# Kernel tuning notes

Measured on AMD Instinct MI355X. Metric: run time of the kernel, lower is better.

## Reference

```python
import math
import jax, jax.numpy as jnp
import numpy as np

B, S, H, D = 8, 2048, 16, 80
DM = H * D  # 1280 = input_dims


def setup_inputs() -> dict:
    key = jax.random.key(0)
    ks = jax.random.split(key, 10)
    s = 0.02
    return {
        "x": jax.random.normal(ks[0], (B, S, DM), dtype=jnp.float32),
        "Wq": jax.random.normal(ks[1], (DM, DM), dtype=jnp.float32) * s,
        "bq": jnp.zeros((DM,), dtype=jnp.float32),
        "Wk": jax.random.normal(ks[2], (DM, DM), dtype=jnp.float32) * s,
        "bk": jnp.zeros((DM,), dtype=jnp.float32),
        "Wv": jax.random.normal(ks[3], (DM, DM), dtype=jnp.float32) * s,
        "bv": jnp.zeros((DM,), dtype=jnp.float32),
        "Wp": jax.random.normal(ks[4], (DM, DM), dtype=jnp.float32) * s,
        "bp": jnp.zeros((DM,), dtype=jnp.float32),
        "per_dim_scale": jnp.ones((D,), dtype=jnp.float32),
    }


def reference(x, Wq, bq, Wk, bk, Wv, bv, Wp, bp, per_dim_scale):
    # Projections: [B,S,DM] -> [B,S,H,D]
    q = (x @ Wq + bq).reshape(B, S, H, D)
    k = (x @ Wk + bk).reshape(B, S, H, D)
    v = (x @ Wv + bv).reshape(B, S, H, D)
    # Faithful to source: matmul over last two dims of (B,S,H,D) tensors,
    # i.e. scores are [B,S,H,H] -- mixing across HEADS at each position.
    scale = 1.0 / math.sqrt(D)
    attn = jnp.einsum('bshd,bstd->bsht', q, k) * scale  # [B,S,H,H]
    attn = jax.nn.softmax(attn, axis=-1)
    out = jnp.einsum('bsht,bstd->bshd', attn, v)  # [B,S,H,D]
    out = out * per_dim_scale  # broadcast over D
    out = out.reshape(B, S, DM)
    return out @ Wp + bp
```

## Files before the change

### kernel.cpp

```cpp
#include <hip/hip_runtime.h>
#include <hip/hip_bf16.h>

#define M_TOT   16384
#define DMODEL  1280
#define NHEAD   16
#define DHEAD   80
#define NTC     5
#define BK      64
#define NKT     (DMODEL / BK)

typedef __attribute__((ext_vector_type(8))) __bf16 bf16x8;
typedef __attribute__((ext_vector_type(4))) float  f32x4;

__device__ __forceinline__ void gload16(const void* g, void* l) {
  __builtin_amdgcn_global_load_lds(
      (const __attribute__((address_space(1))) void*)g,
      (__attribute__((address_space(3))) void*)l, 16, 0, 0);
}

__device__ __forceinline__ float bf2f(unsigned short u) {
  return __uint_as_float((unsigned)u << 16);
}

__global__ __launch_bounds__(256) void cvt_bf16_kernel(
    const float* __restrict__ x, __hip_bfloat16* __restrict__ y, int n4) {
  int i = blockIdx.x * 256 + threadIdx.x;
  if (i >= n4) return;
  float4 v = ((const float4*)x)[i];
  union { ushort4 u; __hip_bfloat16 h[4]; } o;
  o.h[0] = __float2bfloat16(v.x);
  o.h[1] = __float2bfloat16(v.y);
  o.h[2] = __float2bfloat16(v.z);
  o.h[3] = __float2bfloat16(v.w);
  ((ushort4*)y)[i] = o.u;
}

__global__ __launch_bounds__(256) void transpose_cvt_kernel(
    const float* __restrict__ W0, const float* __restrict__ W1,
    const float* __restrict__ W2, const float* __restrict__ W3,
    const float* __restrict__ pds,
    __hip_bfloat16* __restrict__ T0, __hip_bfloat16* __restrict__ T1,
    __hip_bfloat16* __restrict__ T2, __hip_bfloat16* __restrict__ T3) {
  const float* W = blockIdx.z == 0 ? W0 : blockIdx.z == 1 ? W1
                 : blockIdx.z == 2 ? W2 : W3;
  __hip_bfloat16* T = blockIdx.z == 0 ? T0 : blockIdx.z == 1 ? T1
                    : blockIdx.z == 2 ? T2 : T3;
  __shared__ float tile[32][33];
  int bx = blockIdx.x * 32, by = blockIdx.y * 32;
  int tx = threadIdx.x, ty = threadIdx.y;
  for (int j = 0; j < 32; j += 8)
    tile[ty + j][tx] = W[(size_t)(by + ty + j) * DMODEL + bx + tx];
  __syncthreads();
  const float scale = (blockIdx.z == 3) ? pds[(by + tx) % DHEAD] : 1.0f;
  for (int j = 0; j < 32; j += 8)
    T[(size_t)(bx + ty + j) * DMODEL + by + tx] =
        __float2bfloat16(tile[tx][ty + j] * scale);
}

#define MFMA16(AF, BF, MB)                                                   \
  do {                                                                       \
    _Pragma("unroll")                                                        \
    for (int j_ = 0; j_ < 4; ++j_) {                                         \
      _Pragma("unroll")                                                      \
      for (int n_ = 0; n_ < 4; ++n_)                                         \
        acc[(MB) + j_][n_] = __builtin_amdgcn_mfma_f32_16x16x32_bf16(        \
            AF[j_], BF[n_], acc[(MB) + j_][n_], 0, 0, 0);                    \
    }                                                                        \
  } while (0)

#define PHASE_TAIL()                                                         \
  __builtin_amdgcn_sched_barrier(0);                                         \
  __builtin_amdgcn_s_barrier();                                              \
  asm volatile("s_waitcnt lgkmcnt(0)" ::: "memory");                         \
  __builtin_amdgcn_sched_barrier(0)

#define PHASE_END()                                                          \
  __builtin_amdgcn_sched_barrier(0);                                         \
  __builtin_amdgcn_s_barrier()

template <bool OUT_BF16>
__global__ __launch_bounds__(512, 2) void gemm_bt_kernel(
    const __hip_bfloat16* __restrict__ A,
    const __hip_bfloat16* __restrict__ Bt0,
    const __hip_bfloat16* __restrict__ Bt1,
    const __hip_bfloat16* __restrict__ Bt2,
    const float* __restrict__ bias0, const float* __restrict__ bias1,
    const float* __restrict__ bias2,
    void* __restrict__ C0, void* __restrict__ C1, void* __restrict__ C2) {
  const int mat   = blockIdx.y / NTC;
  const int ntile = blockIdx.y % NTC;
  const __hip_bfloat16* Bt = mat == 0 ? Bt0 : mat == 1 ? Bt1 : Bt2;
  const float* bias        = mat == 0 ? bias0 : mat == 1 ? bias1 : bias2;
  void* C                  = mat == 0 ? C0 : mat == 1 ? C1 : C2;

  const int bm = blockIdx.x * 256;
  const int bn = ntile * 256;

  __shared__ __align__(16) char SLDS[131072];

  const int tid  = threadIdx.x;
  const int lane = tid & 63;
  const int wid  = tid >> 6;
  const int wm   = (wid >> 2) * 128;
  const int wn   = (wid & 3) * 64;
  const int lrow = lane & 15;
  const int l4   = lane >> 4;

  const int rsub  = lane >> 2;
  const int cswz  = (lane & 3) ^ ((rsub >> 1) & 3);
  const char* gsrc[2][2][2];
#pragma unroll
  for (int i = 0; i < 2; ++i) {
    const int rA = bm + wid * 32 + i * 16 + rsub;
    const int rB = bn + wid * 32 + i * 16 + rsub;
#pragma unroll
    for (int s = 0; s < 2; ++s) {
      gsrc[0][i][s] = (const char*)A  + (size_t)rA * (DMODEL * 2) + s * 64 + cswz * 16;
      gsrc[1][i][s] = (const char*)Bt + (size_t)rB * (DMODEL * 2) + s * 64 + cswz * 16;
    }
  }

  auto issueGroup = [&](int M, int s, int nbuf, size_t koff) {
    char* d = SLDS + M * 65536 + nbuf * 32768 + s * 16384 + wid * 2048;
    gload16(gsrc[M][0][s] + koff, d);
    gload16(gsrc[M][1][s] + koff, d + 1024);
  };

  f32x4 acc[8][4];
#pragma unroll
  for (int i = 0; i < 8; ++i)
#pragma unroll
    for (int j = 0; j < 4; ++j) acc[i][j] = (f32x4){0.f, 0.f, 0.f, 0.f};

  const int swz  = ((l4 ^ ((lrow >> 1) & 3)) << 4);
  const int aOff = (wm + lrow) * 64 + swz;
  const int bOff = 65536 + (wn + lrow) * 64 + swz;

  issueGroup(0, 0, 0, 0);
  issueGroup(1, 0, 0, 0);
  issueGroup(0, 1, 0, 0);
  issueGroup(1, 1, 0, 0);
  asm volatile("s_waitcnt vmcnt(4)" ::: "memory");
  __builtin_amdgcn_s_barrier();

  for (int t = 0; t < NKT; ++t) {
    const int buf = t & 1, nbuf = buf ^ 1;
    const int b0 = buf << 15;
    const size_t koff = (size_t)(t + 1) * (BK * 2);
    const bool pf = (t + 1 < NKT);

    bf16x8 aF[4], aG[4], bF[4];

#pragma unroll
    for (int j = 0; j < 4; ++j)
      aF[j] = *(const bf16x8*)(const void*)(SLDS + b0 + aOff + j * 1024);
#pragma unroll
    for (int n = 0; n < 4; ++n)
      bF[n] = *(const bf16x8*)(const void*)(SLDS + b0 + bOff + n * 1024);
    if (pf) issueGroup(0, 0, nbuf, koff);
    PHASE_TAIL();
    __builtin_amdgcn_s_setprio(1);
    MFMA16(aF, bF, 0);
    __builtin_amdgcn_s_setprio(0);
    PHASE_END();

#pragma unroll
    for (int j = 0; j < 4; ++j)
      aG[j] = *(const bf16x8*)(const void*)(SLDS + b0 + aOff + (4 + j) * 1024);
    if (pf) {
      issueGroup(1, 0, nbuf, koff);
      asm volatile("s_waitcnt vmcnt(4)" ::: "memory");
    } else {
      asm volatile("s_waitcnt vmcnt(0)" ::: "memory");
    }
    PHASE_TAIL();
    __builtin_amdgcn_s_setprio(1);
    MFMA16(aG, bF, 4);
    __builtin_amdgcn_s_setprio(0);
    PHASE_END();

#pragma unroll
    for (int j = 0; j < 4; ++j)
      aF[j] = *(const bf16x8*)(const void*)(SLDS + b0 + 16384 + aOff + j * 1024);
#pragma unroll
    for (int n = 0; n < 4; ++n)
      bF[n] = *(const bf16x8*)(const void*)(SLDS + b0 + 16384 + bOff + n * 1024);
    if (pf) issueGroup(0, 1, nbuf, koff);
    PHASE_TAIL();
    __builtin_amdgcn_s_setprio(1);
    MFMA16(aF, bF, 0);
    __builtin_amdgcn_s_setprio(0);
    PHASE_END();

#pragma unroll
    for (int j = 0; j < 4; ++j)
      aG[j] = *(const bf16x8*)(const void*)(SLDS + b0 + 16384 + aOff + (4 + j) * 1024);
    if (pf) {
      issueGroup(1, 1, nbuf, koff);
      asm volatile("s_waitcnt vmcnt(4)" ::: "memory");
    }
    PHASE_TAIL();
    __builtin_amdgcn_s_setprio(1);
    MFMA16(aG, bF, 4);
    __builtin_amdgcn_s_setprio(0);
    PHASE_END();
  }

  const int rbase = l4 * 4;
#pragma unroll
  for (int mi = 0; mi < 8; ++mi) {
#pragma unroll
    for (int ni = 0; ni < 4; ++ni) {
      const int col = bn + wn + ni * 16 + lrow;
      const float b2 = bias[col];
#pragma unroll
      for (int r = 0; r < 4; ++r) {
        const int row = bm + wm + mi * 16 + rbase + r;
        const float val = acc[mi][ni][r] + b2;
        if (OUT_BF16)
          ((__hip_bfloat16*)C)[(size_t)row * DMODEL + col] = __float2bfloat16(val);
        else
          ((float*)C)[(size_t)row * DMODEL + col] = val;
      }
    }
  }
}

__global__ __launch_bounds__(256, 2) void gemm_bt128_kernel(
    const __hip_bfloat16* __restrict__ A,
    const __hip_bfloat16* __restrict__ Bt,
    const float* __restrict__ bias,
    float* __restrict__ C) {
  const int bm = blockIdx.x * 128;
  const int bn = blockIdx.y * 128;

  __shared__ __align__(16) char SLDS[65536];

  const int tid  = threadIdx.x;
  const int lane = tid & 63;
  const int wid  = tid >> 6;
  const int wm   = (wid >> 1) * 64;
  const int wn   = (wid & 1) * 64;
  const int lrow = lane & 15;
  const int l4   = lane >> 4;

  const int rsub  = lane >> 2;
  const int cswz  = (lane & 3) ^ ((rsub >> 1) & 3);
  const char* gsrc[2][2][2];
#pragma unroll
  for (int i = 0; i < 2; ++i) {
    const int rA = bm + wid * 32 + i * 16 + rsub;
    const int rB = bn + wid * 32 + i * 16 + rsub;
#pragma unroll
    for (int s = 0; s < 2; ++s) {
      gsrc[0][i][s] = (const char*)A  + (size_t)rA * (DMODEL * 2) + s * 64 + cswz * 16;
      gsrc[1][i][s] = (const char*)Bt + (size_t)rB * (DMODEL * 2) + s * 64 + cswz * 16;
    }
  }

  auto issueGroup = [&](int M, int s, int nbuf, size_t koff) {
    char* d = SLDS + M * 32768 + nbuf * 16384 + s * 8192 + wid * 2048;
    gload16(gsrc[M][0][s] + koff, d);
    gload16(gsrc[M][1][s] + koff, d + 1024);
  };

  f32x4 acc[4][4];
#pragma unroll
  for (int i = 0; i < 4; ++i)
#pragma unroll
    for (int j = 0; j < 4; ++j) acc[i][j] = (f32x4){0.f, 0.f, 0.f, 0.f};

  const int swz  = ((l4 ^ ((lrow >> 1) & 3)) << 4);
  const int aOff = (wm + lrow) * 64 + swz;
  const int bOff = 32768 + (wn + lrow) * 64 + swz;

  issueGroup(0, 0, 0, 0);
  issueGroup(1, 0, 0, 0);
  issueGroup(0, 1, 0, 0);
  issueGroup(1, 1, 0, 0);

  for (int t = 0; t < NKT; ++t) {
    const int buf = t & 1, nbuf = buf ^ 1;
    const int b0 = buf << 14;
    const size_t koff = (size_t)(t + 1) * (BK * 2);
    const bool pf = (t + 1 < NKT);

    asm volatile("s_waitcnt vmcnt(4)" ::: "memory");
    __builtin_amdgcn_s_barrier();
    bf16x8 aF[4], bF[4];
#pragma unroll
    for (int j = 0; j < 4; ++j)
      aF[j] = *(const bf16x8*)(const void*)(SLDS + b0 + aOff + j * 1024);
#pragma unroll
    for (int n = 0; n < 4; ++n)
      bF[n] = *(const bf16x8*)(const void*)(SLDS + b0 + bOff + n * 1024);
    if (pf) { issueGroup(0, 0, nbuf, koff); issueGroup(1, 0, nbuf, koff); }
    __builtin_amdgcn_sched_barrier(0);
    __builtin_amdgcn_s_setprio(1);
    MFMA16(aF, bF, 0);
    __builtin_amdgcn_s_setprio(0);
    __builtin_amdgcn_sched_barrier(0);

    if (pf) asm volatile("s_waitcnt vmcnt(4)" ::: "memory");
    else    asm volatile("s_waitcnt vmcnt(0)" ::: "memory");
    __builtin_amdgcn_s_barrier();
#pragma unroll
    for (int j = 0; j < 4; ++j)
      aF[j] = *(const bf16x8*)(const void*)(SLDS + b0 + 8192 + aOff + j * 1024);
#pragma unroll
    for (int n = 0; n < 4; ++n)
      bF[n] = *(const bf16x8*)(const void*)(SLDS + b0 + 8192 + bOff + n * 1024);
    if (pf) { issueGroup(0, 1, nbuf, koff); issueGroup(1, 1, nbuf, koff); }
    __builtin_amdgcn_sched_barrier(0);
    __builtin_amdgcn_s_setprio(1);
    MFMA16(aF, bF, 0);
    __builtin_amdgcn_s_setprio(0);
    __builtin_amdgcn_sched_barrier(0);
  }

  const int rbase = l4 * 4;
#pragma unroll
  for (int mi = 0; mi < 4; ++mi) {
#pragma unroll
    for (int ni = 0; ni < 4; ++ni) {
      const int col = bn + wn + ni * 16 + lrow;
      const float bb = bias[col];
#pragma unroll
      for (int r = 0; r < 4; ++r) {
        const int row = bm + wm + mi * 16 + rbase + r;
        C[(size_t)row * DMODEL + col] = acc[mi][ni][r] + bb;
      }
    }
  }
}

__global__ __launch_bounds__(512) void attn_kernel(
    const __hip_bfloat16* __restrict__ q, const __hip_bfloat16* __restrict__ k,
    const __hip_bfloat16* __restrict__ v,
    __hip_bfloat16* __restrict__ out) {
  const int half = threadIdx.x >> 8;
  const int tid  = threadIdx.x & 255;
  const size_t base = ((size_t)blockIdx.x * 2 + half) * DMODEL;
  __shared__ float qs[2][16][84], ks[2][16][84], vs[2][16][84];
  __shared__ float ps[2][16][17];

  for (int c = tid; c < 480; c += 256) {
    int matid = c / 160, idx = c - matid * 160;
    int h = idx / 10, d0 = (idx - h * 10) * 8;
    const __hip_bfloat16* src = matid == 0 ? q : matid == 1 ? k : v;
    union { bf16x8 v8; unsigned short u[8]; } uu;
    uu.v8 = *(const bf16x8*)(const void*)(src + base + (size_t)idx * 8);
    float* dst = (matid == 0 ? &qs[half][0][0] : matid == 1 ? &ks[half][0][0]
                                               : &vs[half][0][0]) + h * 84 + d0;
#pragma unroll
    for (int j = 0; j < 8; ++j) dst[j] = bf2f(uu.u[j]);
  }
  __syncthreads();

  const int h = tid >> 4, t = tid & 15;
  float s = 0.f;
#pragma unroll
  for (int d = 0; d < DHEAD; ++d) s += qs[half][h][d] * ks[half][t][d];
  s *= 0.11180339887498948f;

  float m = s;
#pragma unroll
  for (int off = 8; off; off >>= 1) m = fmaxf(m, __shfl_xor(m, off, 16));
  float e = expf(s - m);
  float sum = e;
#pragma unroll
  for (int off = 8; off; off >>= 1) sum += __shfl_xor(sum, off, 16);
  ps[half][h][t] = e / sum;
  __syncthreads();

  {
    const int hh   = tid >> 4;
    const int dloc = (tid & 15) * 5;
    float o[5];
#pragma unroll
    for (int j = 0; j < 5; ++j) o[j] = 0.f;
#pragma unroll
    for (int tt = 0; tt < 16; ++tt) {
      const float p = ps[half][hh][tt];
#pragma unroll
      for (int j = 0; j < 5; ++j) o[j] += p * vs[half][tt][dloc + j];
    }
    __hip_bfloat16* ob = out + base + (size_t)hh * DHEAD + dloc;
#pragma unroll
    for (int j = 0; j < 5; ++j) ob[j] = __float2bfloat16(o[j]);
  }
}

extern "C" void kernel_launch(void* const* d_in, const int* in_sizes, int n_in,
                              void* d_out, int out_size, void* d_ws, size_t ws_size,
                              hipStream_t stream) {
  const float* x   = (const float*)d_in[0];
  const float* Wq  = (const float*)d_in[1];
  const float* bq  = (const float*)d_in[2];
  const float* Wk  = (const float*)d_in[3];
  const float* bk  = (const float*)d_in[4];
  const float* Wv  = (const float*)d_in[5];
  const float* bv  = (const float*)d_in[6];
  const float* Wp  = (const float*)d_in[7];
  const float* bp  = (const float*)d_in[8];
  const float* pds = (const float*)d_in[9];
  float* out = (float*)d_out;

  char* ws = (char*)d_ws;
  const size_t ACT = (size_t)M_TOT * DMODEL * 2;
  const size_t WT  = (size_t)DMODEL * DMODEL * 2;
  __hip_bfloat16* xbf = (__hip_bfloat16*)(ws);
  __hip_bfloat16* qbf = (__hip_bfloat16*)(ws + ACT);
  __hip_bfloat16* kbf = (__hip_bfloat16*)(ws + 2 * ACT);
  __hip_bfloat16* vbf = (__hip_bfloat16*)(ws + 3 * ACT);
  __hip_bfloat16* wtq = (__hip_bfloat16*)(ws + 4 * ACT);
  __hip_bfloat16* wtk = (__hip_bfloat16*)(ws + 4 * ACT + WT);
  __hip_bfloat16* wtv = (__hip_bfloat16*)(ws + 4 * ACT + 2 * WT);
  __hip_bfloat16* wtp = (__hip_bfloat16*)(ws + 4 * ACT + 3 * WT);
  __hip_bfloat16* attnbf = xbf;

  {
    int n4 = (M_TOT * DMODEL) / 4;
    cvt_bf16_kernel<<<n4 / 256, 256, 0, stream>>>(x, xbf, n4);
  }
  {
    dim3 g(DMODEL / 32, DMODEL / 32, 4), b(32, 8);
    transpose_cvt_kernel<<<g, b, 0, stream>>>(Wq, Wk, Wv, Wp, pds,
                                              wtq, wtk, wtv, wtp);
  }
  {
    dim3 g(M_TOT / 256, 3 * NTC);
    gemm_bt_kernel<true><<<g, 512, 0, stream>>>(
        xbf, wtq, wtk, wtv, bq, bk, bv, (void*)qbf, (void*)kbf, (void*)vbf);
  }
  attn_kernel<<<M_TOT / 2, 512, 0, stream>>>(qbf, kbf, vbf, attnbf);
  {
    dim3 g(M_TOT / 128, DMODEL / 128);
    gemm_bt128_kernel<<<g, 256, 0, stream>>>(attnbf, wtp, bp, out);
  }
}
```

Before: 312.5 us.

## Restructure GEMM main loop into 32-wide k-steps with triple-buffered A

Replaces the four-phase double-buffered k-loop with one barrier per 32-wide k-step, using a 3-deep ring for A tiles and a 2-deep ring for B tiles in LDS. LDS use drops from 128KB to 80KB per block, and the per-phase barriers and waits are merged into a single barrier and lgkm wait per step. The goal is less synchronisation overhead and better latency hiding from the deeper prefetch. The trade-off is that each step now holds all eight A fragments in registers at once, which raises register pressure.

Result: no change. 315.7 us (+1.0%).

```diff
diff --git a/kernel.cpp b/kernel.cpp
--- a/kernel.cpp
+++ b/kernel.cpp
@@ -8,6 +8,7 @@
 #define NTC     5
 #define BK      64
 #define NKT     (DMODEL / BK)
+#define NKU     40
 
 typedef __attribute__((ext_vector_type(8))) __bf16 bf16x8;
 typedef __attribute__((ext_vector_type(4))) float  f32x4;
@@ -68,16 +69,6 @@
     }                                                                        \
   } while (0)
 
-#define PHASE_TAIL()                                                         \
-  __builtin_amdgcn_sched_barrier(0);                                         \
-  __builtin_amdgcn_s_barrier();                                              \
-  asm volatile("s_waitcnt lgkmcnt(0)" ::: "memory");                         \
-  __builtin_amdgcn_sched_barrier(0)
-
-#define PHASE_END()                                                          \
-  __builtin_amdgcn_sched_barrier(0);                                         \
-  __builtin_amdgcn_s_barrier()
-
 template <bool OUT_BF16>
 __global__ __launch_bounds__(512, 2) void gemm_bt_kernel(
     const __hip_bfloat16* __restrict__ A,
@@ -96,7 +87,7 @@
   const int bm = blockIdx.x * 256;
   const int bn = ntile * 256;
 
-  __shared__ __align__(16) char SLDS[131072];
+  __shared__ __align__(16) char SLDS[81920];
 
   const int tid  = threadIdx.x;
   const int lane = tid & 63;
@@ -106,24 +97,26 @@
   const int lrow = lane & 15;
   const int l4   = lane >> 4;
 
-  const int rsub  = lane >> 2;
-  const int cswz  = (lane & 3) ^ ((rsub >> 1) & 3);
-  const char* gsrc[2][2][2];
-#pragma unroll
-  for (int i = 0; i < 2; ++i) {
-    const int rA = bm + wid * 32 + i * 16 + rsub;
-    const int rB = bn + wid * 32 + i * 16 + rsub;
-#pragma unroll
-    for (int s = 0; s < 2; ++s) {
-      gsrc[0][i][s] = (const char*)A  + (size_t)rA * (DMODEL * 2) + s * 64 + cswz * 16;
-      gsrc[1][i][s] = (const char*)Bt + (size_t)rB * (DMODEL * 2) + s * 64 + cswz * 16;
-    }
-  }
-
-  auto issueGroup = [&](int M, int s, int nbuf, size_t koff) {
-    char* d = SLDS + M * 65536 + nbuf * 32768 + s * 16384 + wid * 2048;
-    gload16(gsrc[M][0][s] + koff, d);
-    gload16(gsrc[M][1][s] + koff, d + 1024);
+  const int rsub = lane >> 2;
+  const int cswz = (lane & 3) ^ ((rsub >> 1) & 3);
+  const char* srcA0 = (const char*)A +
+      (size_t)(bm + wid * 32 + rsub) * (DMODEL * 2) + cswz * 16;
+  const char* srcA1 = srcA0 + 16 * (DMODEL * 2);
+  const char* srcB0 = (const char*)Bt +
+      (size_t)(bn + wid * 32 + rsub) * (DMODEL * 2) + cswz * 16;
+  const char* srcB1 = srcB0 + 16 * (DMODEL * 2);
+
+  auto stageA = [&](int v) {
+    char* d = SLDS + (v % 3) * 16384 + wid * 2048;
+    const size_t ko = (size_t)v * 64;
+    gload16(srcA0 + ko, d);
+    gload16(srcA1 + ko, d + 1024);
+  };
+  auto stageB = [&](int v) {
+    char* d = SLDS + 49152 + (v & 1) * 16384 + wid * 2048;
+    const size_t ko = (size_t)v * 64;
+    gload16(srcB0 + ko, d);
+    gload16(srcB1 + ko, d + 1024);
   };
 
   f32x4 acc[8][4];
@@ -134,76 +127,35 @@
 
   const int swz  = ((l4 ^ ((lrow >> 1) & 3)) << 4);
   const int aOff = (wm + lrow) * 64 + swz;
-  const int bOff = 65536 + (wn + lrow) * 64 + swz;
-
-  issueGroup(0, 0, 0, 0);
-  issueGroup(1, 0, 0, 0);
-  issueGroup(0, 1, 0, 0);
-  issueGroup(1, 1, 0, 0);
-  asm volatile("s_waitcnt vmcnt(4)" ::: "memory");
-  __builtin_amdgcn_s_barrier();
-
-  for (int t = 0; t < NKT; ++t) {
-    const int buf = t & 1, nbuf = buf ^ 1;
-    const int b0 = buf << 15;
-    const size_t koff = (size_t)(t + 1) * (BK * 2);
-    const bool pf = (t + 1 < NKT);
-
-    bf16x8 aF[4], aG[4], bF[4];
-
-#pragma unroll
-    for (int j = 0; j < 4; ++j)
-      aF[j] = *(const bf16x8*)(const void*)(SLDS + b0 + aOff + j * 1024);
+  const int bOff = (wn + lrow) * 64 + swz;
+
+  stageA(0);
+  stageB(0);
+  stageA(1);
+
+  for (int u = 0; u < NKU; ++u) {
+    if (u < NKU - 1) asm volatile("s_waitcnt vmcnt(2)" ::: "memory");
+    else             asm volatile("s_waitcnt vmcnt(0)" ::: "memory");
+    __builtin_amdgcn_s_barrier();
+    if (u + 1 < NKU) stageB(u + 1);
+    if (u + 2 < NKU) stageA(u + 2);
+
+    const char* as = SLDS + (u % 3) * 16384;
+    const char* bs = SLDS + 49152 + (u & 1) * 16384;
+    bf16x8 aF[8], bF[4];
+#pragma unroll
+    for (int j = 0; j < 8; ++j)
+      aF[j] = *(const bf16x8*)(const void*)(as + aOff + j * 1024);
 #pragma unroll
     for (int n = 0; n < 4; ++n)
-      bF[n] = *(const bf16x8*)(const void*)(SLDS + b0 + bOff + n * 1024);
-    if (pf) issueGroup(0, 0, nbuf, koff);
-    PHASE_TAIL();
+      bF[n] = *(const bf16x8*)(const void*)(bs + bOff + n * 1024);
+    asm volatile("s_waitcnt lgkmcnt(0)" ::: "memory");
+    __builtin_amdgcn_sched_barrier(0);
     __builtin_amdgcn_s_setprio(1);
     MFMA16(aF, bF, 0);
+    MFMA16((aF + 4), bF, 4);
     __builtin_amdgcn_s_setprio(0);
-    PHASE_END();
-
-#pragma unroll
-    for (int j = 0; j < 4; ++j)
-      aG[j] = *(const bf16x8*)(const void*)(SLDS + b0 + aOff + (4 + j) * 1024);
-    if (pf) {
-      issueGroup(1, 0, nbuf, koff);
-      asm volatile("s_waitcnt vmcnt(4)" ::: "memory");
-    } else {
-      asm volatile("s_waitcnt vmcnt(0)" ::: "memory");
-    }
-    PHASE_TAIL();
-    __builtin_amdgcn_s_setprio(1);
-    MFMA16(aG, bF, 4);
-    __builtin_amdgcn_s_setprio(0);
-    PHASE_END();
-
-#pragma unroll
-    for (int j = 0; j < 4; ++j)
-      aF[j] = *(const bf16x8*)(const void*)(SLDS + b0 + 16384 + aOff + j * 1024);
-#pragma unroll
-    for (int n = 0; n < 4; ++n)
-      bF[n] = *(const bf16x8*)(const void*)(SLDS + b0 + 16384 + bOff + n * 1024);
-    if (pf) issueGroup(0, 1, nbuf, koff);
-    PHASE_TAIL();
-    __builtin_amdgcn_s_setprio(1);
-    MFMA16(aF, bF, 0);
-    __builtin_amdgcn_s_setprio(0);
-    PHASE_END();
-
-#pragma unroll
-    for (int j = 0; j < 4; ++j)
-      aG[j] = *(const bf16x8*)(const void*)(SLDS + b0 + 16384 + aOff + (4 + j) * 1024);
-    if (pf) {
-      issueGroup(1, 1, nbuf, koff);
-      asm volatile("s_waitcnt vmcnt(4)" ::: "memory");
-    }
-    PHASE_TAIL();
-    __builtin_amdgcn_s_setprio(1);
-    MFMA16(aG, bF, 4);
-    __builtin_amdgcn_s_setprio(0);
-    PHASE_END();
+    __builtin_amdgcn_sched_barrier(0);
   }
 
   const int rbase = l4 * 4;
```
